# Kernel optimization log

Measured on AMD Instinct MI355X. Metric: run time of the kernel, lower is better.

Reference implementation:

```python
import jax, jax.numpy as jnp
import numpy as np
import math

HEADS = 16
SPH = 64      # size_per_head
KEY = 64      # key_size (defaults to size_per_head)
EMB = 1024
STEP = 3


def extract_seq_patches(x, kernel_size, step):
    # x: [B, L, D] -> [B, L, kernel_size, D]; patch j at pos t is x_pad[t - p_left + j*step]
    B, L, D = x.shape
    k_size = kernel_size + (step - 1) * (kernel_size - 1)
    p_right = (k_size - 1) // 2
    p_left = k_size - 1 - p_right
    xp = jnp.pad(x, ((0, 0), (p_left, p_right), (0, 0)))
    xs = [xp[:, i:i + L] for i in range(0, k_size, step)]  # kernel_size slices
    return jnp.stack(xs, axis=2)


def setup_inputs() -> dict:
    key = jax.random.key(0)
    kx, kq, kk, kv = jax.random.split(key, 4)
    B, L = 2, 4096
    x = jax.random.normal(kx, (B, L, EMB), dtype=jnp.float32)
    W_q = jax.random.normal(kq, (EMB, HEADS * KEY), dtype=jnp.float32) * 0.02
    W_k = jax.random.normal(kk, (EMB, HEADS * KEY), dtype=jnp.float32) * 0.02
    W_v = jax.random.normal(kv, (EMB, HEADS * SPH), dtype=jnp.float32) * 0.02
    return {"x": x, "W_q": W_q, "W_k": W_k, "W_v": W_v}


def _forward(x, W_q, W_k, W_v):
    B, L, D = x.shape
    pad_len = STEP - L % STEP
    x = jnp.pad(x, ((0, 0), (0, pad_len), (0, 0)))
    new_len = L + pad_len
    blocks = new_len // STEP
    q = x @ W_q  # [B, new_len, H*KEY]
    k = x @ W_k
    v = x @ W_v
    ksz = 1 + 2 * (STEP - 1)  # kernel_size = 5
    kp = extract_seq_patches(k, ksz, STEP)  # [B, new_len, ksz, H*KEY]
    vp = extract_seq_patches(v, ksz, STEP)
    # reshape to [B, H, step, blocks, d]
    q = q.reshape(B, blocks, STEP, HEADS, KEY).transpose(0, 3, 2, 1, 4)
    kb = k.reshape(B, blocks, STEP, HEADS, KEY).transpose(0, 3, 2, 1, 4)
    vb = v.reshape(B, blocks, STEP, HEADS, SPH).transpose(0, 3, 2, 1, 4)
    # neighbor patches: [B, H, step, blocks, ksz, d]
    kp = kp.reshape(B, blocks, STEP, ksz, HEADS, KEY).transpose(0, 4, 2, 1, 3, 5)
    vp = vp.reshape(B, blocks, STEP, ksz, HEADS, SPH).transpose(0, 4, 2, 1, 3, 5)
    scale = 1.0 / math.sqrt(KEY)
    # strided attention over blocks (same residue mod step): [B,H,step,blocks,blocks]
    a = jnp.einsum('bhsqk,bhspk->bhsqp', q, kb) * scale
    # block-local neighbor attention: [B,H,step,blocks,ksz]
    ap = jnp.einsum('bhsqk,bhsqnk->bhsqn', q, kp) * scale
    A = jax.nn.softmax(jnp.concatenate([a, ap], axis=-1), axis=-1)
    a, ap = A[..., :blocks], A[..., blocks:]
    o = (jnp.einsum('bhsqp,bhspd->bhsqd', a, vb)
         + jnp.einsum('bhsqn,bhsqnd->bhsqd', ap, vp))
    o = o.transpose(0, 3, 2, 1, 4).reshape(B, new_len, HEADS * SPH)
    return o[:, :L]


def reference(x, W_q, W_k, W_v):
    return _forward(x, W_q, W_k, W_v)
```

## Files before the change

### kernel.cpp

```cpp
#include <hip/hip_runtime.h>
#include <hip/hip_bf16.h>

typedef unsigned int u32;
typedef unsigned short u16;
typedef short s8v __attribute__((ext_vector_type(8)));
typedef short s4v __attribute__((ext_vector_type(4)));
typedef float f4v __attribute__((ext_vector_type(4)));
typedef u32 u32x2 __attribute__((ext_vector_type(2)));

#define NBLK 1366
#define VROW 1376
#define QSCALE 0.18033688011112042f

__device__ __forceinline__ u16 f2b(float f) {
  u32 u = __builtin_bit_cast(u32, f);
  u = (u + 0x7FFFu + ((u >> 16) & 1u)) >> 16;
  return (u16)u;
}

__device__ __forceinline__ u32 cvtpk(float a, float b) {
  u32 r;
  asm("v_cvt_pk_bf16_f32 %0, %1, %2" : "=v"(r) : "v"(a), "v"(b));
  return r;
}

__device__ __forceinline__ float fexp2(float x) {
#if defined(__has_builtin)
#if __has_builtin(__builtin_amdgcn_exp2f)
  return __builtin_amdgcn_exp2f(x);
#define FEXP2_DONE 1
#endif
#endif
#ifndef FEXP2_DONE
  float r;
  asm("v_exp_f32 %0, %1" : "=v"(r) : "v"(x));
  return r;
#endif
}

__device__ __forceinline__ void gll16(const void* g, void* l) {
  __builtin_amdgcn_global_load_lds(
      (const __attribute__((address_space(1))) u32*)g,
      (__attribute__((address_space(3))) u32*)l, 16, 0, 0);
}

__device__ __forceinline__ f4v mfma32(s8v a, s8v b, f4v c) {
  return __builtin_amdgcn_mfma_f32_16x16x32_bf16(a, b, c, 0, 0, 0);
}

__device__ __forceinline__ f4v mfma16(s4v a, s4v b, f4v c) {
#if defined(__has_builtin)
#if __has_builtin(__builtin_amdgcn_mfma_f32_16x16x16bf16_1k)
#define MFMA16_BUILTIN 1
#endif
#endif
#ifdef MFMA16_BUILTIN
  return __builtin_amdgcn_mfma_f32_16x16x16bf16_1k(a, b, c, 0, 0, 0);
#else
  f4v d;
  asm("v_mfma_f32_16x16x16_bf16 %0, %1, %2, %3" : "=v"(d) : "v"(a), "v"(b), "v"(c));
  return d;
#endif
}

__global__ __launch_bounds__(256) void k_convert_x(const float* __restrict__ x,
                                                   u16* __restrict__ xb) {
  int gid = blockIdx.x * 256 + threadIdx.x;
  long base = (long)gid * 8;
  if (base >= 8320L * 1024L) return;
  int m = (int)(base >> 10);
  int c = (int)(base & 1023);
  int b = m / 4098;
  int t = m - b * 4098;
  s8v pack;
  if (m < 8196 && t < 4096) {
    const float* src = x + ((size_t)b * 4096 + t) * 1024 + c;
    float4 v0 = *(const float4*)(src);
    float4 v1 = *(const float4*)(src + 4);
    pack[0] = (short)f2b(v0.x); pack[1] = (short)f2b(v0.y);
    pack[2] = (short)f2b(v0.z); pack[3] = (short)f2b(v0.w);
    pack[4] = (short)f2b(v1.x); pack[5] = (short)f2b(v1.y);
    pack[6] = (short)f2b(v1.z); pack[7] = (short)f2b(v1.w);
  } else {
#pragma unroll
    for (int i = 0; i < 8; ++i) pack[i] = 0;
  }
  *(s8v*)(xb + base) = pack;
}

__global__ __launch_bounds__(256) void k_transpose_w(const float* __restrict__ Wq,
                                                     const float* __restrict__ Wk,
                                                     const float* __restrict__ Wv,
                                                     u16* __restrict__ Wt) {
  const float* W = (blockIdx.z == 0) ? Wq : ((blockIdx.z == 1) ? Wk : Wv);
  u16* dst = Wt + (size_t)blockIdx.z * 1024 * 1024;
  __shared__ float tile[32][33];
  int n0 = blockIdx.x * 32, k0 = blockIdx.y * 32;
  int tx = threadIdx.x, ty = threadIdx.y;
#pragma unroll
  for (int i = 0; i < 4; ++i)
    tile[ty + i * 8][tx] = W[(size_t)(k0 + ty + i * 8) * 1024 + n0 + tx];
  __syncthreads();
#pragma unroll
  for (int i = 0; i < 4; ++i)
    dst[(size_t)(n0 + ty + i * 8) * 1024 + k0 + tx] = f2b(tile[tx][ty + i * 8]);
}

__global__ __launch_bounds__(256) void k_gemm_qkv(const u16* __restrict__ xb,
                                                  const u16* __restrict__ Wt,
                                                  u16* __restrict__ Qp,
                                                  u16* __restrict__ Kp,
                                                  u16* __restrict__ Vt) {
  const int zid = blockIdx.z;
  const int m0 = blockIdx.x * 128;
  const int n0 = blockIdx.y * 128;
  const u16* Bg = Wt + (size_t)zid * 1024 * 1024 + (size_t)n0 * 1024;

  __shared__ __align__(16) u16 shl[16384];
  u16* A0 = shl;
  u16* A1 = shl + 4096;
  u16* B0 = shl + 8192;
  u16* B1 = shl + 12288;

  const int tid = threadIdx.x;
  const int lane = tid & 63;
  const int w = tid >> 6;
  const int wr = w >> 1, wc = w & 1;
  const int lo = lane & 15, g = lane >> 4;

  const int lrow = lane >> 2;
  const int csrc = (lane & 3) ^ ((lane >> 3) & 3);
  const int rsw = (g ^ ((lo >> 1) & 3)) << 4;

  f4v acc[4][4];
#pragma unroll
  for (int i = 0; i < 4; ++i)
#pragma unroll
    for (int j = 0; j < 4; ++j) {
      f4v z = {0.f, 0.f, 0.f, 0.f};
      acc[i][j] = z;
    }

  auto stage = [&](int kt, u16* Ab, u16* Bb) {
#pragma unroll
    for (int c = 0; c < 2; ++c) {
      int rloc = w * 32 + c * 16 + lrow;
      gll16(xb + (size_t)(m0 + rloc) * 1024 + kt + csrc * 8,
            Ab + (w * 32 + c * 16) * 32);
      gll16(Bg + (size_t)rloc * 1024 + kt + csrc * 8,
            Bb + (w * 32 + c * 16) * 32);
    }
  };

  auto compute = [&](const u16* Ab, const u16* Bb) {
    s8v af[4], bf[4];
#pragma unroll
    for (int i = 0; i < 4; ++i) {
      int ar = wr * 64 + i * 16 + lo;
      af[i] = *(const s8v*)((const char*)Ab + ar * 64 + rsw);
      int br = wc * 64 + i * 16 + lo;
      bf[i] = *(const s8v*)((const char*)Bb + br * 64 + rsw);
    }
    __builtin_amdgcn_s_setprio(1);
#pragma unroll
    for (int i = 0; i < 4; ++i)
#pragma unroll
      for (int j = 0; j < 4; ++j)
        acc[i][j] = mfma32(af[i], bf[j], acc[i][j]);
    __builtin_amdgcn_s_setprio(0);
  };

#define BAR_VM4                                             \
  asm volatile("s_waitcnt vmcnt(4)" ::: "memory");          \
  __builtin_amdgcn_s_barrier();                             \
  asm volatile("" ::: "memory");
#define BAR_LGKM                                            \
  asm volatile("s_waitcnt lgkmcnt(0)" ::: "memory");        \
  __builtin_amdgcn_s_barrier();                             \
  asm volatile("" ::: "memory");

  stage(0, A0, B0);
#pragma unroll 1
  for (int kk = 0; kk < 15; ++kk) {
    int kt = kk * 64;
    stage(kt + 32, A1, B1);
    BAR_VM4
    compute(A0, B0);
    BAR_LGKM
    stage(kt + 64, A0, B0);
    BAR_VM4
    compute(A1, B1);
    BAR_LGKM
  }
  stage(31 * 32, A1, B1);
  BAR_VM4
  compute(A0, B0);
  BAR_LGKM
  asm volatile("s_waitcnt vmcnt(0)" ::: "memory");
  __builtin_amdgcn_s_barrier();
  asm volatile("" ::: "memory");
  compute(A1, B1);
  __syncthreads();

#undef BAR_VM4
#undef BAR_LGKM

  const float esc = (zid == 0) ? QSCALE : 1.0f;
  if (zid != 2) {
    u16* dq = (zid == 0) ? Qp : Kp;
#pragma unroll
    for (int i = 0; i < 4; ++i) {
#pragma unroll
      for (int r = 0; r < 4; ++r) {
        int m = m0 + wr * 64 + i * 16 + g * 4 + r;
        if (m >= 8196) continue;
        int b = m / 4098;
        int t = m - b * 4098;
        int s = t % 3;
        int p = t / 3;
        int cb = (b * 3 + s) * 16;
#pragma unroll
        for (int j = 0; j < 4; ++j) {
          int n = n0 + wc * 64 + j * 16 + lo;
          int h = n >> 6, d = n & 63;
          dq[(size_t)((cb + h) * NBLK + p) * 64 + d] = f2b(acc[i][j][r] * esc);
        }
      }
    }
  } else {
    u16* tile = shl;
#pragma unroll
    for (int i = 0; i < 4; ++i)
#pragma unroll
      for (int r = 0; r < 4; ++r) {
        int ml = wr * 64 + i * 16 + g * 4 + r;
#pragma unroll
        for (int j = 0; j < 4; ++j) {
          int nl = wc * 64 + j * 16 + lo;
          tile[ml * 128 + nl] = f2b(acc[i][j][r]);
        }
      }
    __syncthreads();
    for (int pair = tid; pair < 384; pair += 256) {
      int nl = pair & 127;
      int s = pair >> 7;
      int n = n0 + nl;
      int h = n >> 6, d = n & 63;
      for (int b = 0; b < 2; ++b) {
        int mlo = m0 > b * 4098 ? m0 : b * 4098;
        int cap = b * 4098 + 4096;
        int mhi = (m0 + 128 < cap) ? m0 + 128 : cap;
        if (mlo >= mhi) continue;
        int t_lo = mlo - b * 4098;
        int add = (s - (t_lo % 3) + 3) % 3;
        int t = t_lo + add;
        int tend = mhi - b * 4098;
        u16* dst = Vt + (size_t)(((b * 3 + s) * 16 + h) * 64 + d) * VROW;
        for (; t < tend; t += 3)
          dst[t / 3] = tile[(b * 4098 + t - m0) * 128 + nl];
      }
    }
  }
}

__global__ __launch_bounds__(256) void k_attn(const u16* __restrict__ Qp,
                                              const u16* __restrict__ Kp,
                                              const u16* __restrict__ Vt,
                                              float* __restrict__ out) {
  const int wg = blockIdx.x;
  const int idx = (wg & 7) * 264 + (wg >> 3);
  const int combo = idx / 22;
  const int q0 = (idx % 22) * 64;
  const int b = combo / 48;
  const int rem = combo - b * 48;
  const int s = rem >> 4;
  const int h = rem & 15;
  const int tid = threadIdx.x, lane = tid & 63, w = tid >> 6;
  const int lo = lane & 15, g = lane >> 4;

  const u16* Qg = Qp + (size_t)combo * (NBLK * 64);
  const u16* Kg = Kp + (size_t)combo * (NBLK * 64);
  const u16* Vg = Vt + (size_t)combo * (64 * VROW);

  __shared__ __align__(16) u16 Kl[64 * 64];
  __shared__ __align__(16) u16 Vl[64 * 64];

  const int pq_e = q0 + w * 16 + lo;
  const int qc = (pq_e < NBLK) ? pq_e : (NBLK - 1);
  s8v qf0 = *(const s8v*)(Qg + (size_t)qc * 64 + g * 8);
  s8v qf1 = *(const s8v*)(Qg + (size_t)qc * 64 + 32 + g * 8);

  s4v onesf;
  onesf[0] = onesf[1] = onesf[2] = onesf[3] = (short)0x3F80;

  f4v oacc[4];
#pragma unroll
  for (int i = 0; i < 4; ++i) {
    f4v z = {0.f, 0.f, 0.f, 0.f};
    oacc[i] = z;
  }
  f4v den_acc = {0.f, 0.f, 0.f, 0.f};

  const int lrow = lane >> 3;
  const int schunk = (lane & 7) ^ lrow;

  for (int j0 = 0; j0 < NBLK; j0 += 64) {
    __syncthreads();
#pragma unroll
    for (int c = 0; c < 2; ++c) {
      int rloc = w * 16 + c * 8 + lrow;
      gll16(Kg + (size_t)(j0 + rloc) * 64 + schunk * 8, Kl + (w * 16 + c * 8) * 64);
      gll16(Vg + (size_t)rloc * VROW + j0 + schunk * 8, Vl + (w * 16 + c * 8) * 64);
    }
    __syncthreads();

    f4v sacc[4];
    __builtin_amdgcn_s_setprio(1);
#pragma unroll
    for (int kb = 0; kb < 4; ++kb) {
      f4v z = {0.f, 0.f, 0.f, 0.f};
      int row = kb * 16 + lo;
      int sw = (row & 7) << 4;
      s8v kf0 = *(const s8v*)((const char*)Kl + row * 128 + ((g * 16) ^ sw));
      s8v kf1 = *(const s8v*)((const char*)Kl + row * 128 + ((64 + g * 16) ^ sw));
      z = mfma32(kf0, qf0, z);
      sacc[kb] = mfma32(kf1, qf1, z);
    }
    __builtin_amdgcn_s_setprio(0);

    s4v ef[4];
    const bool special = (j0 >= q0 - 64 && j0 <= q0 + 64) || (j0 + 64 > NBLK);
    if (special) {
#pragma unroll
      for (int kb = 0; kb < 4; ++kb) {
        float e[4];
#pragma unroll
        for (int r = 0; r < 4; ++r) {
          int j = j0 + kb * 16 + g * 4 + r;
          float ev = fexp2(sacc[kb][r]);
          int dd = j - pq_e;
          float fac = (j < NBLK) ? (((dd <= 2) && (dd >= -2)) ? 2.f : 1.f) : 0.f;
          e[r] = ev * fac;
        }
        u32x2 w2;
        w2[0] = cvtpk(e[0], e[1]);
        w2[1] = cvtpk(e[2], e[3]);
        ef[kb] = __builtin_bit_cast(s4v, w2);
      }
    } else {
#pragma unroll
      for (int kb = 0; kb < 4; ++kb) {
        u32x2 w2;
        w2[0] = cvtpk(fexp2(sacc[kb][0]), fexp2(sacc[kb][1]));
        w2[1] = cvtpk(fexp2(sacc[kb][2]), fexp2(sacc[kb][3]));
        ef[kb] = __builtin_bit_cast(s4v, w2);
      }
    }

    __builtin_amdgcn_s_setprio(1);
#pragma unroll
    for (int kb = 0; kb < 4; ++kb)
      den_acc = mfma16(ef[kb], onesf, den_acc);
#pragma unroll
    for (int db = 0; db < 4; ++db) {
      int row = db * 16 + lo;
      int sw = (row & 7) << 4;
#pragma unroll
      for (int kb = 0; kb < 4; ++kb) {
        s4v vf = *(const s4v*)((const char*)Vl + row * 128 + ((kb * 32 + g * 8) ^ sw));
        oacc[db] = mfma16(ef[kb], vf, oacc[db]);
      }
    }
    __builtin_amdgcn_s_setprio(0);
  }

  const int hbase = h * 64;
#pragma unroll
  for (int r = 0; r < 4; ++r) {
    int pq = q0 + w * 16 + g * 4 + r;
    float dden = den_acc[r];
    dden += (pq == 0 || pq == NBLK - 1) ? 2.f : ((pq == 1 || pq == NBLK - 2) ? 1.f : 0.f);
    float rr = 1.f / dden;
    int t = 3 * pq + s;
    if (pq < NBLK && t < 4096) {
      float* orow = out + ((size_t)b * 4096 + t) * 1024 + hbase;
#pragma unroll
      for (int db = 0; db < 4; ++db)
        orow[db * 16 + lo] = oacc[db][r] * rr;
    }
  }
}

extern "C" void kernel_launch(void* const* d_in, const int* in_sizes, int n_in,
                              void* d_out, int out_size, void* d_ws, size_t ws_size,
                              hipStream_t stream) {
  const float* x  = (const float*)d_in[0];
  const float* Wq = (const float*)d_in[1];
  const float* Wk = (const float*)d_in[2];
  const float* Wv = (const float*)d_in[3];
  float* out = (float*)d_out;

  u16* ws = (u16*)d_ws;
  u16* xb = ws;
  u16* Wt = xb + 8519680;
  u16* Qp = Wt + 3145728;
  u16* Kp = Qp + 8392704;
  u16* Vt = Kp + 8392704;

  k_convert_x<<<4160, 256, 0, stream>>>(x, xb);
  k_transpose_w<<<dim3(32, 32, 3), dim3(32, 8), 0, stream>>>(Wq, Wk, Wv, Wt);
  hipMemsetAsync(Vt, 0, (size_t)(8454144 + 256) * sizeof(u16), stream);
  k_gemm_qkv<<<dim3(65, 8, 3), 256, 0, stream>>>(xb, Wt, Qp, Kp, Vt);
  k_attn<<<dim3(2112), 256, 0, stream>>>(Qp, Kp, Vt, out);
}
```

Before: 218.7 us.

## Switch attention to 32x32 MFMA with 128-query tiles and fuse prep kernels

```diff
diff --git a/kernel.cpp b/kernel.cpp
--- a/kernel.cpp
+++ b/kernel.cpp
@@ -6,6 +6,7 @@
 typedef short s8v __attribute__((ext_vector_type(8)));
 typedef short s4v __attribute__((ext_vector_type(4)));
 typedef float f4v __attribute__((ext_vector_type(4)));
+typedef float f16v __attribute__((ext_vector_type(16)));
 typedef u32 u32x2 __attribute__((ext_vector_type(2)));
 
 #define NBLK 1366
@@ -48,62 +49,81 @@
   return __builtin_amdgcn_mfma_f32_16x16x32_bf16(a, b, c, 0, 0, 0);
 }
 
-__device__ __forceinline__ f4v mfma16(s4v a, s4v b, f4v c) {
+__device__ __forceinline__ f16v mfma3216(s8v a, s8v b, f16v c) {
+  return __builtin_amdgcn_mfma_f32_32x32x16_bf16(a, b, c, 0, 0, 0);
+}
+
+__device__ __forceinline__ f16v mfma3208(s4v a, s4v b, f16v c) {
 #if defined(__has_builtin)
-#if __has_builtin(__builtin_amdgcn_mfma_f32_16x16x16bf16_1k)
-#define MFMA16_BUILTIN 1
-#endif
-#endif
-#ifdef MFMA16_BUILTIN
-  return __builtin_amdgcn_mfma_f32_16x16x16bf16_1k(a, b, c, 0, 0, 0);
+#if __has_builtin(__builtin_amdgcn_mfma_f32_32x32x8bf16_1k)
+#define MFMA3208_BUILTIN 1
+#endif
+#endif
+#ifdef MFMA3208_BUILTIN
+  return __builtin_amdgcn_mfma_f32_32x32x8bf16_1k(a, b, c, 0, 0, 0);
 #else
-  f4v d;
-  asm("v_mfma_f32_16x16x16_bf16 %0, %1, %2, %3" : "=v"(d) : "v"(a), "v"(b), "v"(c));
+  f16v d;
+  asm("v_mfma_f32_32x32x8_bf16 %0, %1, %2, %3" : "=v"(d) : "v"(a), "v"(b), "v"(c));
   return d;
 #endif
 }
 
-__global__ __launch_bounds__(256) void k_convert_x(const float* __restrict__ x,
-                                                   u16* __restrict__ xb) {
-  int gid = blockIdx.x * 256 + threadIdx.x;
-  long base = (long)gid * 8;
-  if (base >= 8320L * 1024L) return;
-  int m = (int)(base >> 10);
-  int c = (int)(base & 1023);
-  int b = m / 4098;
-  int t = m - b * 4098;
-  s8v pack;
-  if (m < 8196 && t < 4096) {
-    const float* src = x + ((size_t)b * 4096 + t) * 1024 + c;
-    float4 v0 = *(const float4*)(src);
-    float4 v1 = *(const float4*)(src + 4);
-    pack[0] = (short)f2b(v0.x); pack[1] = (short)f2b(v0.y);
-    pack[2] = (short)f2b(v0.z); pack[3] = (short)f2b(v0.w);
-    pack[4] = (short)f2b(v1.x); pack[5] = (short)f2b(v1.y);
-    pack[6] = (short)f2b(v1.z); pack[7] = (short)f2b(v1.w);
+__global__ __launch_bounds__(256) void k_prep(const float* __restrict__ x,
+                                              const float* __restrict__ Wq,
+                                              const float* __restrict__ Wk,
+                                              const float* __restrict__ Wv,
+                                              u16* __restrict__ xb,
+                                              u16* __restrict__ Wt,
+                                              u16* __restrict__ Vt) {
+  const int bid = blockIdx.x;
+  const int tid = threadIdx.x;
+  if (bid < 4160) {
+    long base = ((long)bid * 256 + tid) * 8;
+    if (base >= 8320L * 1024L) return;
+    int m = (int)(base >> 10);
+    int c = (int)(base & 1023);
+    int b = m / 4098;
+    int t = m - b * 4098;
+    s8v pack;
+    if (m < 8196 && t < 4096) {
+      const float* src = x + ((size_t)b * 4096 + t) * 1024 + c;
+      float4 v0 = *(const float4*)(src);
+      float4 v1 = *(const float4*)(src + 4);
+      pack[0] = (short)f2b(v0.x); pack[1] = (short)f2b(v0.y);
+      pack[2] = (short)f2b(v0.z); pack[3] = (short)f2b(v0.w);
+      pack[4] = (short)f2b(v1.x); pack[5] = (short)f2b(v1.y);
+      pack[6] = (short)f2b(v1.z); pack[7] = (short)f2b(v1.w);
+    } else {
+#pragma unroll
+      for (int i = 0; i < 8; ++i) pack[i] = 0;
+    }
+    *(s8v*)(xb + base) = pack;
+  } else if (bid < 7232) {
+    __shared__ float tile[32][33];
+    int bid3 = bid - 4160;
+    int z = bid3 >> 10;
+    int rem = bid3 & 1023;
+    const float* W = (z == 0) ? Wq : ((z == 1) ? Wk : Wv);
+    u16* dst = Wt + (size_t)z * 1024 * 1024;
+    int n0 = (rem & 31) * 32, k0 = (rem >> 5) * 32;
+    int tx = tid & 31, ty = tid >> 5;
+#pragma unroll
+    for (int i = 0; i < 4; ++i)
+      tile[ty + i * 8][tx] = W[(size_t)(k0 + ty + i * 8) * 1024 + n0 + tx];
+    __syncthreads();
+#pragma unroll
+    for (int i = 0; i < 4; ++i)
+      dst[(size_t)(n0 + ty + i * 8) * 1024 + k0 + tx] = f2b(tile[tx][ty + i * 8]);
   } else {
-#pragma unroll
-    for (int i = 0; i < 8; ++i) pack[i] = 0;
+    int gidx = (bid - 7232) * 256 + tid;
+    if (gidx < 6144) {
+      u16* dst = Vt + (size_t)gidx * VROW + NBLK;
+#pragma unroll
+      for (int i = 0; i < 10; ++i) dst[i] = 0;
+    } else if (gidx < 6400) {
+      Vt[(size_t)6144 * VROW + (gidx - 6144)] = 0;
+    }
   }
-  *(s8v*)(xb + base) = pack;
-}
-
-__global__ __launch_bounds__(256) void k_transpose_w(const float* __restrict__ Wq,
-                                                     const float* __restrict__ Wk,
-                                                     const float* __restrict__ Wv,
-                                                     u16* __restrict__ Wt) {
-  const float* W = (blockIdx.z == 0) ? Wq : ((blockIdx.z == 1) ? Wk : Wv);
-  u16* dst = Wt + (size_t)blockIdx.z * 1024 * 1024;
-  __shared__ float tile[32][33];
-  int n0 = blockIdx.x * 32, k0 = blockIdx.y * 32;
-  int tx = threadIdx.x, ty = threadIdx.y;
-#pragma unroll
-  for (int i = 0; i < 4; ++i)
-    tile[ty + i * 8][tx] = W[(size_t)(k0 + ty + i * 8) * 1024 + n0 + tx];
-  __syncthreads();
-#pragma unroll
-  for (int i = 0; i < 4; ++i)
-    dst[(size_t)(n0 + ty + i * 8) * 1024 + k0 + tx] = f2b(tile[tx][ty + i * 8]);
 }
 
 __global__ __launch_bounds__(256) void k_gemm_qkv(const u16* __restrict__ xb,
@@ -263,20 +283,20 @@
   }
 }
 
-__global__ __launch_bounds__(256) void k_attn(const u16* __restrict__ Qp,
-                                              const u16* __restrict__ Kp,
-                                              const u16* __restrict__ Vt,
-                                              float* __restrict__ out) {
+__global__ __launch_bounds__(256, 4) void k_attn(const u16* __restrict__ Qp,
+                                                 const u16* __restrict__ Kp,
+                                                 const u16* __restrict__ Vt,
+                                                 float* __restrict__ out) {
   const int wg = blockIdx.x;
-  const int idx = (wg & 7) * 264 + (wg >> 3);
-  const int combo = idx / 22;
-  const int q0 = (idx % 22) * 64;
+  const int idx = (wg & 7) * 132 + (wg >> 3);
+  const int combo = idx / 11;
+  const int qb = idx - combo * 11;
   const int b = combo / 48;
   const int rem = combo - b * 48;
   const int s = rem >> 4;
   const int h = rem & 15;
   const int tid = threadIdx.x, lane = tid & 63, w = tid >> 6;
-  const int lo = lane & 15, g = lane >> 4;
+  const int lq = lane & 31, lh = lane >> 5;
 
   const u16* Qg = Qp + (size_t)combo * (NBLK * 64);
   const u16* Kg = Kp + (size_t)combo * (NBLK * 64);
@@ -285,108 +305,106 @@
   __shared__ __align__(16) u16 Kl[64 * 64];
   __shared__ __align__(16) u16 Vl[64 * 64];
 
-  const int pq_e = q0 + w * 16 + lo;
-  const int qc = (pq_e < NBLK) ? pq_e : (NBLK - 1);
-  s8v qf0 = *(const s8v*)(Qg + (size_t)qc * 64 + g * 8);
-  s8v qf1 = *(const s8v*)(Qg + (size_t)qc * 64 + 32 + g * 8);
+  const int qg = qb * 128 + w * 32 + lq;
+  const int qc = (qg < NBLK) ? qg : (NBLK - 1);
+  s8v qf[4];
+#pragma unroll
+  for (int ss = 0; ss < 4; ++ss)
+    qf[ss] = *(const s8v*)(Qg + (size_t)qc * 64 + ss * 16 + lh * 8);
 
   s4v onesf;
   onesf[0] = onesf[1] = onesf[2] = onesf[3] = (short)0x3F80;
 
-  f4v oacc[4];
-#pragma unroll
-  for (int i = 0; i < 4; ++i) {
-    f4v z = {0.f, 0.f, 0.f, 0.f};
-    oacc[i] = z;
-  }
-  f4v den_acc = {0.f, 0.f, 0.f, 0.f};
-
-  const int lrow = lane >> 3;
-  const int schunk = (lane & 7) ^ lrow;
+  f16v oacc0, oacc1, den_acc;
+#pragma unroll
+  for (int i = 0; i < 16; ++i) { oacc0[i] = 0.f; oacc1[i] = 0.f; den_acc[i] = 0.f; }
+
+  const int srow8 = lane >> 3;
+  const int schunk = ((lane & 7) - srow8) & 7;
+  const int qmin = qb * 128;
 
   for (int j0 = 0; j0 < NBLK; j0 += 64) {
     __syncthreads();
 #pragma unroll
     for (int c = 0; c < 2; ++c) {
-      int rloc = w * 16 + c * 8 + lrow;
-      gll16(Kg + (size_t)(j0 + rloc) * 64 + schunk * 8, Kl + (w * 16 + c * 8) * 64);
-      gll16(Vg + (size_t)rloc * VROW + j0 + schunk * 8, Vl + (w * 16 + c * 8) * 64);
+      int rbase = c * 32 + w * 8;
+      gll16(Kg + (size_t)(j0 + rbase + srow8) * 64 + schunk * 8, Kl + rbase * 64);
+      gll16(Vg + (size_t)(rbase + srow8) * VROW + j0 + schunk * 8, Vl + rbase * 64);
     }
     __syncthreads();
 
-    f4v sacc[4];
-    __builtin_amdgcn_s_setprio(1);
-#pragma unroll
-    for (int kb = 0; kb < 4; ++kb) {
-      f4v z = {0.f, 0.f, 0.f, 0.f};
-      int row = kb * 16 + lo;
-      int sw = (row & 7) << 4;
-      s8v kf0 = *(const s8v*)((const char*)Kl + row * 128 + ((g * 16) ^ sw));
-      s8v kf1 = *(const s8v*)((const char*)Kl + row * 128 + ((64 + g * 16) ^ sw));
-      z = mfma32(kf0, qf0, z);
-      sacc[kb] = mfma32(kf1, qf1, z);
-    }
-    __builtin_amdgcn_s_setprio(0);
-
-    s4v ef[4];
-    const bool special = (j0 >= q0 - 64 && j0 <= q0 + 64) || (j0 + 64 > NBLK);
-    if (special) {
-#pragma unroll
-      for (int kb = 0; kb < 4; ++kb) {
-        float e[4];
-#pragma unroll
-        for (int r = 0; r < 4; ++r) {
-          int j = j0 + kb * 16 + g * 4 + r;
-          float ev = fexp2(sacc[kb][r]);
-          int dd = j - pq_e;
+    const bool special = ((j0 <= qmin + 129) && (j0 + 65 >= qmin)) || (j0 + 64 > NBLK);
+    s4v ef[8];
+#pragma unroll
+    for (int jb = 0; jb < 2; ++jb) {
+      f16v sacc;
+#pragma unroll
+      for (int i = 0; i < 16; ++i) sacc[i] = 0.f;
+      __builtin_amdgcn_s_setprio(1);
+#pragma unroll
+      for (int ss = 0; ss < 4; ++ss) {
+        s8v kf = *(const s8v*)((const char*)Kl + (jb * 32 + lq) * 128 +
+                               ((((ss * 2 + lh) + (lq & 7)) & 7) << 4));
+        sacc = mfma3216(kf, qf[ss], sacc);
+      }
+      __builtin_amdgcn_s_setprio(0);
+
+      if (special) {
+        float e[16];
+#pragma unroll
+        for (int r = 0; r < 16; ++r) {
+          int j = j0 + jb * 32 + (r & 3) + 8 * (r >> 2) + 4 * lh;
+          float ev = fexp2(sacc[r]);
+          int dd = j - qg;
           float fac = (j < NBLK) ? (((dd <= 2) && (dd >= -2)) ? 2.f : 1.f) : 0.f;
           e[r] = ev * fac;
         }
-        u32x2 w2;
-        w2[0] = cvtpk(e[0], e[1]);
-        w2[1] = cvtpk(e[2], e[3]);
-        ef[kb] = __builtin_bit_cast(s4v, w2);
+#pragma unroll
+        for (int k4 = 0; k4 < 4; ++k4) {
+          u32x2 w2;
+          w2[0] = cvtpk(e[k4 * 4 + 0], e[k4 * 4 + 1]);
+          w2[1] = cvtpk(e[k4 * 4 + 2], e[k4 * 4 + 3]);
+          ef[jb * 4 + k4] = __builtin_bit_cast(s4v, w2);
+        }
+      } else {
+#pragma unroll
+        for (int k4 = 0; k4 < 4; ++k4) {
+          u32x2 w2;
+          w2[0] = cvtpk(fexp2(sacc[k4 * 4 + 0]), fexp2(sacc[k4 * 4 + 1]));
+          w2[1] = cvtpk(fexp2(sacc[k4 * 4 + 2]), fexp2(sacc[k4 * 4 + 3]));
+          ef[jb * 4 + k4] = __builtin_bit_cast(s4v, w2);
+        }
       }
-    } else {
-#pragma unroll
-      for (int kb = 0; kb < 4; ++kb) {
-        u32x2 w2;
-        w2[0] = cvtpk(fexp2(sacc[kb][0]), fexp2(sacc[kb][1]));
-        w2[1] = cvtpk(fexp2(sacc[kb][2]), fexp2(sacc[kb][3]));
-        ef[kb] = __builtin_bit_cast(s4v, w2);
-      }
     }
 
     __builtin_amdgcn_s_setprio(1);
 #pragma unroll
-    for (int kb = 0; kb < 4; ++kb)
-      den_acc = mfma16(ef[kb], onesf, den_acc);
-#pragma unroll
-    for (int db = 0; db < 4; ++db) {
-      int row = db * 16 + lo;
-      int sw = (row & 7) << 4;
-#pragma unroll
-      for (int kb = 0; kb < 4; ++kb) {
-        s4v vf = *(const s4v*)((const char*)Vl + row * 128 + ((kb * 32 + g * 8) ^ sw));
-        oacc[db] = mfma16(ef[kb], vf, oacc[db]);
-      }
+    for (int ks = 0; ks < 8; ++ks)
+      den_acc = mfma3208(ef[ks], onesf, den_acc);
+#pragma unroll
+    for (int ks = 0; ks < 8; ++ks) {
+      const char* vb = (const char*)Vl + lq * 128 +
+                       (((ks + (lq & 7)) & 7) << 4) + lh * 8;
+      s4v vf0 = *(const s4v*)(vb);
+      s4v vf1 = *(const s4v*)(vb + 32 * 128);
+      oacc0 = mfma3208(ef[ks], vf0, oacc0);
+      oacc1 = mfma3208(ef[ks], vf1, oacc1);
     }
     __builtin_amdgcn_s_setprio(0);
   }
 
   const int hbase = h * 64;
 #pragma unroll
-  for (int r = 0; r < 4; ++r) {
-    int pq = q0 + w * 16 + g * 4 + r;
+  for (int r = 0; r < 16; ++r) {
+    int q = qb * 128 + w * 32 + (r & 3) + 8 * (r >> 2) + 4 * lh;
     float dden = den_acc[r];
-    dden += (pq == 0 || pq == NBLK - 1) ? 2.f : ((pq == 1 || pq == NBLK - 2) ? 1.f : 0.f);
+    dden += (q == 0 || q == NBLK - 1) ? 2.f : ((q == 1 || q == NBLK - 2) ? 1.f : 0.f);
     float rr = 1.f / dden;
-    int t = 3 * pq + s;
-    if (pq < NBLK && t < 4096) {
-      float* orow = out + ((size_t)b * 4096 + t) * 1024 + hbase;
-#pragma unroll
-      for (int db = 0; db < 4; ++db)
-        orow[db * 16 + lo] = oacc[db][r] * rr;
+    int t = 3 * q + s;
+    if (q < NBLK && t < 4096) {
+      float* orow = out + ((size_t)b * 4096 + t) * 1024 + hbase + lq;
+      orow[0] = oacc0[r] * rr;
+      orow[32] = oacc1[r] * rr;
     }
   }
 }
@@ -407,9 +425,7 @@
   u16* Kp = Qp + 8392704;
   u16* Vt = Kp + 8392704;
 
-  k_convert_x<<<4160, 256, 0, stream>>>(x, xb);
-  k_transpose_w<<<dim3(32, 32, 3), dim3(32, 8), 0, stream>>>(Wq, Wk, Wv, Wt);
-  hipMemsetAsync(Vt, 0, (size_t)(8454144 + 256) * sizeof(u16), stream);
+  k_prep<<<dim3(7257), 256, 0, stream>>>(x, Wq, Wk, Wv, xb, Wt, Vt);
   k_gemm_qkv<<<dim3(65, 8, 3), 256, 0, stream>>>(xb, Wt, Qp, Kp, Vt);
-  k_attn<<<dim3(2112), 256, 0, stream>>>(Qp, Kp, Vt, out);
-}
+  k_attn<<<dim3(1056), 256, 0, stream>>>(Qp, Kp, Vt, out);
+}
```

Measured after the change: 223.2 us. 1.02x slower.
